# Performance work log

Measured on AMD Instinct MI355X. Metric: run time of the kernel, lower is better.

The kernel has to match this reference:

```python
import jax, jax.numpy as jnp
import numpy as np
from jax import lax

B, T, H, W, C = 32, 250, 28, 28, 1
CLASSES, IPC = 25, 10
UNITS = 512
MEM_CELLS = CLASSES * IPC  # 250
CELL = 64
HEADS = 4
FEAT = 2 * 2 * 32          # conv output flattened = 128
XDIM = FEAT + CLASSES      # 153
IN_LSTM = XDIM + HEADS * CELL  # 409
EPS_BN = 1e-3


def setup_inputs() -> dict:
    key = jax.random.key(0)
    ks = iter(jax.random.split(key, 40))
    s = 0.02
    d = {}
    d['images'] = jax.random.normal(next(ks), (B, T, H, W, C), jnp.float32)
    d['previous_labels'] = jax.random.randint(next(ks), (B, T), 0, CLASSES, jnp.int32)
    # conv stack
    for i, (ci, co) in enumerate([(1, 8), (8, 16), (16, 32)], start=1):
        d[f'k{i}'] = jax.random.normal(next(ks), (3, 3, ci, co), jnp.float32) * s
        d[f'cb{i}'] = jnp.zeros((co,), jnp.float32)
        d[f'g{i}'] = jnp.ones((co,), jnp.float32)
        d[f'be{i}'] = jnp.zeros((co,), jnp.float32)
        d[f'mm{i}'] = jnp.zeros((co,), jnp.float32)
        d[f'mv{i}'] = jnp.ones((co,), jnp.float32)
    # LSTM cell (keras gate order i,f,g,o)
    d['Wx'] = jax.random.normal(next(ks), (IN_LSTM, 4 * UNITS), jnp.float32) * s
    d['Wh'] = jax.random.normal(next(ks), (UNITS, 4 * UNITS), jnp.float32) * s
    d['bl'] = jnp.zeros((4 * UNITS,), jnp.float32)
    # parameters dense -> (read_heads+1)*cell_size, tanh
    d['Wp'] = jax.random.normal(next(ks), (UNITS, (HEADS + 1) * CELL), jnp.float32) * s
    d['bp'] = jnp.zeros(((HEADS + 1) * CELL,), jnp.float32)
    # output layer: Dense(units, tanh) on concat(h, read_value)
    d['Wo'] = jax.random.normal(next(ks), (UNITS + HEADS * CELL, UNITS), jnp.float32) * s
    d['bo'] = jnp.zeros((UNITS,), jnp.float32)
    # final classifier
    d['Wf'] = jax.random.normal(next(ks), (UNITS, CLASSES), jnp.float32) * s
    d['bf'] = jnp.zeros((CLASSES,), jnp.float32)
    return d


def _conv_bn_relu(x, k, cb, g, be, mm, mv):
    y = lax.conv_general_dilated(x, k, (2, 2), 'VALID',
                                 dimension_numbers=('NHWC', 'HWIO', 'NHWC')) + cb
    y = (y - mm) * g * lax.rsqrt(mv + EPS_BN) + be  # inference BN
    return jax.nn.relu(y)


def _l2n(x):
    return x * lax.rsqrt(jnp.maximum(jnp.sum(x * x, axis=-1, keepdims=True), 1e-12))


def _forward(images, previous_labels, k1, cb1, g1, be1, mm1, mv1,
             k2, cb2, g2, be2, mm2, mv2, k3, cb3, g3, be3, mm3, mv3,
             Wx, Wh, bl, Wp, bp, Wo, bo, Wf, bf):
    x = images.reshape(B * T, H, W, C)
    x = _conv_bn_relu(x, k1, cb1, g1, be1, mm1, mv1)
    x = _conv_bn_relu(x, k2, cb2, g2, be2, mm2, mv2)
    x = _conv_bn_relu(x, k3, cb3, g3, be3, mm3, mv3)
    x = x.reshape(B, T, FEAT)
    oh = jax.nn.one_hot(previous_labels, CLASSES, dtype=x.dtype)
    x = jnp.concatenate([x, oh], axis=-1)  # [B, T, XDIM]

    def step(carry, xt):
        h, c, rv, mem = carry
        inp = jnp.concatenate([xt, rv], axis=-1)
        z = inp @ Wx + h @ Wh + bl
        zi, zf, zg, zo = jnp.split(z, 4, axis=-1)
        i, f, g = jax.nn.sigmoid(zi), jax.nn.sigmoid(zf), jnp.tanh(zg)
        o = jax.nn.sigmoid(zo)
        c = f * c + i * g
        h = o * jnp.tanh(c)
        hid = jnp.tanh(h @ Wp + bp)
        wv = hid[:, :CELL]                                # write value
        keys = hid[:, CELL:].reshape(B, HEADS, CELL)
        att = jnp.einsum('brs,bms->brm', _l2n(keys), _l2n(mem))
        w = jax.nn.softmax(att, axis=-1)
        rv = jnp.einsum('brm,bms->brs', w, mem).reshape(B, HEADS * CELL)
        mem = jnp.concatenate([wv[:, None, :], mem[:, :-1]], axis=1)  # shift write
        out = jnp.tanh(jnp.concatenate([h, rv], axis=-1) @ Wo + bo)
        return (h, c, rv, mem), out

    carry0 = (jnp.zeros((B, UNITS)), jnp.zeros((B, UNITS)),
              jnp.zeros((B, HEADS * CELL)), jnp.zeros((B, MEM_CELLS, CELL)))
    _, ys = lax.scan(step, carry0, jnp.swapaxes(x, 0, 1))  # ys: [T, B, UNITS]
    rnn_out = jnp.swapaxes(ys, 0, 1)
    return jax.nn.softmax(rnn_out @ Wf + bf, axis=-1)


def reference(images, previous_labels, k1, cb1, g1, be1, mm1, mv1,
              k2, cb2, g2, be2, mm2, mv2, k3, cb3, g3, be3, mm3, mv3,
              Wx, Wh, bl, Wp, bp, Wo, bo, Wf, bf):
    return _forward(images, previous_labels, k1, cb1, g1, be1, mm1, mv1,
                    k2, cb2, g2, be2, mm2, mv2, k3, cb3, g3, be3, mm3, mv3,
                    Wx, Wh, bl, Wp, bp, Wo, bo, Wf, bf)
```

## Files before the change

### kernel.cpp

```cpp
#include <hip/hip_runtime.h>


constexpr size_t OFF_FEATP  = 0;
constexpr size_t OFF_WXI    = OFF_FEATP + (size_t)8000 * 128;
constexpr size_t OFF_WHI    = OFF_WXI + (size_t)409 * 2048;
constexpr size_t OFF_BLI    = OFF_WHI + (size_t)512 * 2048;
constexpr size_t OFF_ZP0    = OFF_BLI + 2048;
constexpr size_t OFF_ZP1    = OFF_ZP0 + 131072;
constexpr size_t OFF_OH0    = OFF_ZP1 + 131072;
constexpr size_t OFF_OH1    = OFF_OH0 + 32768;
constexpr size_t OFF_HP0    = OFF_OH1 + 32768;
constexpr size_t OFF_HP1    = OFF_HP0 + 10240;
constexpr size_t OFF_OUTPRE = OFF_HP1 + 10240;
constexpr size_t OFF_HT     = OFF_OUTPRE + 16384;
constexpr size_t OFF_RVT    = OFF_HT + 32768;
constexpr size_t OFF_BAR    = OFF_RVT + 16384;
constexpr size_t OFF_WPT    = OFF_BAR + 4096;
constexpr size_t WS_FLOATS  = OFF_WPT + (size_t)163840;

constexpr size_t OFF_HTT = OFF_ZP1;
constexpr size_t OFF_WVP = OFF_ZP1 + 32768;

constexpr int DYN_FLOATS = 34816;
constexpr int DYN_BYTES  = DYN_FLOATS * 4;

constexpr int CZP = 0, CHT = 512, COH = 1024, CWV = 1536, CRV = 2048,
              COP = 2560, CCO = 3072, CRING = 3584;

__device__ __forceinline__ float sigm(float x) { return 1.f / (1.f + __expf(-x)); }

__device__ __forceinline__ void st_sc(float* p, float v) {
  __hip_atomic_store(p, v, __ATOMIC_RELAXED, __HIP_MEMORY_SCOPE_AGENT);
}
__device__ __forceinline__ float ld_sc(const float* p) {
  return __hip_atomic_load(p, __ATOMIC_RELAXED, __HIP_MEMORY_SCOPE_AGENT);
}
__device__ __forceinline__ void ld8x2_sc(const double* b0, double* v) {
  const double *p0 = b0, *p1 = b0 + 512, *p2 = b0 + 1024, *p3 = b0 + 1536,
               *p4 = b0 + 2048, *p5 = b0 + 2560, *p6 = b0 + 3072, *p7 = b0 + 3584;
  asm volatile(
      "global_load_dwordx2 %0, %8, off sc0 sc1\n\t"
      "global_load_dwordx2 %1, %9, off sc0 sc1\n\t"
      "global_load_dwordx2 %2, %10, off sc0 sc1\n\t"
      "global_load_dwordx2 %3, %11, off sc0 sc1\n\t"
      "global_load_dwordx2 %4, %12, off sc0 sc1\n\t"
      "global_load_dwordx2 %5, %13, off sc0 sc1\n\t"
      "global_load_dwordx2 %6, %14, off sc0 sc1\n\t"
      "global_load_dwordx2 %7, %15, off sc0 sc1\n\t"
      "s_waitcnt vmcnt(0)"
      : "=&v"(v[0]), "=&v"(v[1]), "=&v"(v[2]), "=&v"(v[3]),
        "=&v"(v[4]), "=&v"(v[5]), "=&v"(v[6]), "=&v"(v[7])
      : "v"(p0), "v"(p1), "v"(p2), "v"(p3), "v"(p4), "v"(p5), "v"(p6), "v"(p7)
      : "memory");
}
__device__ __forceinline__ void ld10x2_sc(const double* b0, const double* z0,
                                          const double* z1, double* v) {
  const double *p0 = b0, *p1 = b0 + 512, *p2 = b0 + 1024, *p3 = b0 + 1536,
               *p4 = b0 + 2048, *p5 = b0 + 2560, *p6 = b0 + 3072, *p7 = b0 + 3584;
  asm volatile(
      "global_load_dwordx2 %0, %10, off sc0 sc1\n\t"
      "global_load_dwordx2 %1, %11, off sc0 sc1\n\t"
      "global_load_dwordx2 %2, %12, off sc0 sc1\n\t"
      "global_load_dwordx2 %3, %13, off sc0 sc1\n\t"
      "global_load_dwordx2 %4, %14, off sc0 sc1\n\t"
      "global_load_dwordx2 %5, %15, off sc0 sc1\n\t"
      "global_load_dwordx2 %6, %16, off sc0 sc1\n\t"
      "global_load_dwordx2 %7, %17, off sc0 sc1\n\t"
      "global_load_dwordx2 %8, %18, off sc0 sc1\n\t"
      "global_load_dwordx2 %9, %19, off sc0 sc1\n\t"
      "s_waitcnt vmcnt(0)"
      : "=&v"(v[0]), "=&v"(v[1]), "=&v"(v[2]), "=&v"(v[3]), "=&v"(v[4]),
        "=&v"(v[5]), "=&v"(v[6]), "=&v"(v[7]), "=&v"(v[8]), "=&v"(v[9])
      : "v"(p0), "v"(p1), "v"(p2), "v"(p3), "v"(p4), "v"(p5), "v"(p6), "v"(p7),
        "v"(z0), "v"(z1)
      : "memory");
}
__device__ __forceinline__ void ldpair_sc(const float* a, const float* b,
                                          float& x, float& y) {
  asm volatile(
      "global_load_dword %0, %2, off sc0 sc1\n\t"
      "global_load_dword %1, %3, off sc0 sc1\n\t"
      "s_waitcnt vmcnt(0)"
      : "=&v"(x), "=&v"(y) : "v"(a), "v"(b) : "memory");
}
__device__ __forceinline__ double ld1x2_sc(const double* a) {
  double x;
  asm volatile(
      "global_load_dwordx2 %0, %1, off sc0 sc1\n\t"
      "s_waitcnt vmcnt(0)"
      : "=&v"(x) : "v"(a) : "memory");
  return x;
}
__device__ __forceinline__ int sum8_bar(const int* b) {
  int v0, v1, v2, v3, v4, v5, v6, v7;
  asm volatile(
      "global_load_dword %0, %8, off sc0 sc1\n\t"
      "global_load_dword %1, %9, off sc0 sc1\n\t"
      "global_load_dword %2, %10, off sc0 sc1\n\t"
      "global_load_dword %3, %11, off sc0 sc1\n\t"
      "global_load_dword %4, %12, off sc0 sc1\n\t"
      "global_load_dword %5, %13, off sc0 sc1\n\t"
      "global_load_dword %6, %14, off sc0 sc1\n\t"
      "global_load_dword %7, %15, off sc0 sc1\n\t"
      "s_waitcnt vmcnt(0)"
      : "=&v"(v0), "=&v"(v1), "=&v"(v2), "=&v"(v3),
        "=&v"(v4), "=&v"(v5), "=&v"(v6), "=&v"(v7)
      : "v"(b), "v"(b + 64), "v"(b + 128), "v"(b + 192),
        "v"(b + 256), "v"(b + 320), "v"(b + 384), "v"(b + 448)
      : "memory");
  return ((v0 + v1) + (v2 + v3)) + ((v4 + v5) + (v6 + v7));
}

__global__ __launch_bounds__(256) void prep_kernel(const float* __restrict__ Wx,
                                                   const float* __restrict__ Wh,
                                                   const float* __restrict__ bl,
                                                   const float* __restrict__ Wp,
                                                   float* __restrict__ ws) {
  float* WXI = ws + OFF_WXI;
  float* WHI = ws + OFF_WHI;
  float* BLI = ws + OFF_BLI;
  float* WPT = ws + OFF_WPT;
  const int t0 = 409 * 2048;
  const int t1 = t0 + 512 * 2048;
  const int t2 = t1 + 2048;
  const int total = t2 + 163840;
  for (int idx = blockIdx.x * blockDim.x + threadIdx.x; idx < total;
       idx += gridDim.x * blockDim.x) {
    if (idx < t0) {
      int k = idx >> 11, cc = idx & 2047;
      WXI[idx] = Wx[(size_t)k * 2048 + (cc & 3) * 512 + (cc >> 2)];
    } else if (idx < t1) {
      int j = idx - t0;
      int k = j >> 11, cc = j & 2047;
      WHI[j] = Wh[(size_t)k * 2048 + (cc & 3) * 512 + (cc >> 2)];
    } else if (idx < t2) {
      int cc = idx - t1;
      BLI[cc] = bl[(cc & 3) * 512 + (cc >> 2)];
    } else {
      int e = idx - t2;
      int k4 = e / 1280, r = e - k4 * 1280;
      int j = r >> 2, ks = r & 3;
      WPT[e] = Wp[(size_t)(k4 * 4 + ks) * 320 + j];
    }
  }
}

__global__ __launch_bounds__(128) void conv_kernel(
    const float* __restrict__ img,
    const float* __restrict__ k1, const float* __restrict__ cb1, const float* __restrict__ g1,
    const float* __restrict__ be1, const float* __restrict__ mm1, const float* __restrict__ mv1,
    const float* __restrict__ k2, const float* __restrict__ cb2, const float* __restrict__ g2,
    const float* __restrict__ be2, const float* __restrict__ mm2, const float* __restrict__ mv2,
    const float* __restrict__ k3, const float* __restrict__ cb3, const float* __restrict__ g3,
    const float* __restrict__ be3, const float* __restrict__ mm3, const float* __restrict__ mv3,
    float* __restrict__ ws) {
  __shared__ float s_in[784];
  __shared__ float s_y1[13 * 13 * 8];
  __shared__ float s_y2[6 * 6 * 16];
  __shared__ float s_k1[72], s_k2[1152], s_k3[4608];
  __shared__ float s_s1[8], s_b1[8], s_s2[16], s_b2[16], s_s3[32], s_b3[32];
  float* FEATP = ws + OFF_FEATP;
  const int n = blockIdx.x, tid = threadIdx.x;
  const float* ip = img + (size_t)n * 784;
  for (int i = tid; i < 784; i += 128) s_in[i] = ip[i];
  for (int i = tid; i < 72; i += 128) s_k1[i] = k1[i];
  for (int i = tid; i < 1152; i += 128) s_k2[i] = k2[i];
  for (int i = tid; i < 4608; i += 128) s_k3[i] = k3[i];
  if (tid < 8) {
    float s = g1[tid] * rsqrtf(mv1[tid] + 1e-3f);
    s_s1[tid] = s; s_b1[tid] = (cb1[tid] - mm1[tid]) * s + be1[tid];
  } else if (tid >= 32 && tid < 48) {
    int c = tid - 32;
    float s = g2[c] * rsqrtf(mv2[c] + 1e-3f);
    s_s2[c] = s; s_b2[c] = (cb2[c] - mm2[c]) * s + be2[c];
  } else if (tid >= 64 && tid < 96) {
    int c = tid - 64;
    float s = g3[c] * rsqrtf(mv3[c] + 1e-3f);
    s_s3[c] = s; s_b3[c] = (cb3[c] - mm3[c]) * s + be3[c];
  }
  __syncthreads();
  for (int idx = tid; idx < 13 * 13 * 8; idx += 128) {
    int co = idx & 7, pos = idx >> 3;
    int j = pos % 13, i = pos / 13;
    float acc = 0.f;
    #pragma unroll
    for (int ky = 0; ky < 3; ++ky)
      #pragma unroll
      for (int kx = 0; kx < 3; ++kx)
        acc += s_in[(2 * i + ky) * 28 + (2 * j + kx)] * s_k1[(ky * 3 + kx) * 8 + co];
    float v = acc * s_s1[co] + s_b1[co];
    s_y1[idx] = v > 0.f ? v : 0.f;
  }
  __syncthreads();
  for (int idx = tid; idx < 6 * 6 * 16; idx += 128) {
    int co = idx & 15, pos = idx >> 4;
    int j = pos % 6, i = pos / 6;
    float acc = 0.f;
    for (int ky = 0; ky < 3; ++ky)
      for (int kx = 0; kx < 3; ++kx) {
        int base = ((2 * i + ky) * 13 + (2 * j + kx)) * 8;
        int kb = (ky * 3 + kx) * 128 + co;
        #pragma unroll
        for (int ci = 0; ci < 8; ++ci) acc += s_y1[base + ci] * s_k2[kb + ci * 16];
      }
    float v = acc * s_s2[co] + s_b2[co];
    s_y2[idx] = v > 0.f ? v : 0.f;
  }
  __syncthreads();
  for (int idx = tid; idx < 128; idx += 128) {
    int co = idx & 31, pos = idx >> 5;
    int j = pos & 1, i = pos >> 1;
    float acc = 0.f;
    for (int ky = 0; ky < 3; ++ky)
      for (int kx = 0; kx < 3; ++kx) {
        int base = ((2 * i + ky) * 6 + (2 * j + kx)) * 16;
        int kb = (ky * 3 + kx) * 512 + co;
        #pragma unroll
        for (int ci = 0; ci < 16; ++ci) acc += s_y2[base + ci] * s_k3[kb + ci * 32];
      }
    float v = acc * s_s3[co] + s_b3[co];
    FEATP[(size_t)n * 128 + idx] = v > 0.f ? v : 0.f;
  }
}

__global__ __launch_bounds__(512) void lstm_kernel(
    const int* __restrict__ labels,
    const float* __restrict__ Wo, const float* __restrict__ bo,
    const float* __restrict__ Wp, const float* __restrict__ bp,
    const float* __restrict__ Wf, const float* __restrict__ bf,
    float* __restrict__ ws, float* __restrict__ out) {
  extern __shared__ float dyn[];
  const float* FEATP = ws + OFF_FEATP;
  const float* WXI   = ws + OFF_WXI;
  const float* WHI   = ws + OFF_WHI;
  const float* BLI   = ws + OFF_BLI;
  float* ZP0    = ws + OFF_ZP0;
  float* OH0    = ws + OFF_OH0;
  float* OH1    = ws + OFF_OH1;
  float* OUTPRE = ws + OFF_OUTPRE;
  float* HT     = ws + OFF_HT;
  float* HTT    = ws + OFF_HTT;
  float* RVT    = ws + OFF_RVT;
  float* WVPp   = ws + OFF_WVP;
  const float* WPT = ws + OFF_WPT;
  int*   BARp   = (int*)(ws + OFF_BAR);

  const int bid = blockIdx.x;
  const int tid = threadIdx.x;

  auto waitC = [&](int base, int target) {
    if (tid == 0) {
      while (sum8_bar(BARp + base) < target) {}
    }
    __syncthreads();
  };
  auto bumpC = [&](int base) {
    asm volatile("s_waitcnt vmcnt(0)" ::: "memory");
    __syncthreads();
    if (tid == 0) atomicAdd(&BARp[base + ((bid & 7) << 6)], 1);
  };

  auto stage_act = [&](float* dst, const float* src) {
    double v[8];
    ld8x2_sc((const double*)src + tid, v);
    #pragma unroll
    for (int j = 0; j < 8; ++j) {
      int i = (tid + j * 512) << 1;
      *(double*)&dst[(i >> 5) * 36 + (i & 31)] = v[j];
    }
  };

  auto E32 = [&](const float* Wm, const float* Am, int K, float* part, float2& r) {
    const int wv = tid >> 6, l = tid & 63;
    const int ksub = l & 1, cg = (l >> 1) & 3, bg = l >> 3;
    const int Kp = K >> 4;
    const int kb = wv * (K >> 3) + ksub * Kp;
    const float* wp = Wm + (size_t)kb * 32 + cg * 8;
    const float* ap = Am + (size_t)kb * 36 + bg * 4;
    float4 acc[8];
    #pragma unroll
    for (int i = 0; i < 8; ++i) acc[i] = {0.f, 0.f, 0.f, 0.f};
    #pragma unroll 4
    for (int kk = 0; kk < Kp; ++kk) {
      float4 w0 = *(const float4*)(wp + kk * 32);
      float4 w1 = *(const float4*)(wp + kk * 32 + 4);
      float4 a  = *(const float4*)(ap + kk * 36);
      float wl[8];
      *(float4*)&wl[0] = w0; *(float4*)&wl[4] = w1;
      #pragma unroll
      for (int i = 0; i < 8; ++i) {
        acc[i].x = fmaf(wl[i], a.x, acc[i].x);
        acc[i].y = fmaf(wl[i], a.y, acc[i].y);
        acc[i].z = fmaf(wl[i], a.z, acc[i].z);
        acc[i].w = fmaf(wl[i], a.w, acc[i].w);
      }
    }
    #pragma unroll
    for (int i = 0; i < 8; ++i) {
      acc[i].x += __shfl_xor(acc[i].x, 1, 64);
      acc[i].y += __shfl_xor(acc[i].y, 1, 64);
      acc[i].z += __shfl_xor(acc[i].z, 1, 64);
      acc[i].w += __shfl_xor(acc[i].w, 1, 64);
    }
    const int ob = (cg * 8) * 36 + bg * 4;
    if (ksub == 0 && wv < 4) {
      float* pb = part + wv * 1152 + ob;
      #pragma unroll
      for (int i = 0; i < 8; ++i) *(float4*)(pb + i * 36) = acc[i];
    }
    __syncthreads();
    if (ksub == 0 && wv >= 4) {
      float* pb = part + (wv - 4) * 1152 + ob;
      #pragma unroll
      for (int i = 0; i < 8; ++i) {
        float4 t = *(float4*)(pb + i * 36);
        t.x += acc[i].x; t.y += acc[i].y; t.z += acc[i].z; t.w += acc[i].w;
        *(float4*)(pb + i * 36) = t;
      }
    }
    __syncthreads();
    const int c = tid & 31, b2 = (tid >> 5) * 2;
    const int o = c * 36 + b2;
    float2 s0 = *(float2*)(part + o);
    float2 s1 = *(float2*)(part + 1152 + o);
    float2 s2 = *(float2*)(part + 2304 + o);
    float2 s3 = *(float2*)(part + 3456 + o);
    r.x = (s0.x + s1.x) + (s2.x + s3.x);
    r.y = (s0.y + s1.y) + (s2.y + s3.y);
  };

  if (bid < 64) {
    const int c0 = bid * 32;
    for (int i = tid; i < 8192; i += 512)
      dyn[i] = WXI[(size_t)(153 + (i >> 5)) * 2048 + c0 + (i & 31)];
    for (int i = tid; i < 4096; i += 512)
      dyn[8192 + i] = WXI[(size_t)(i >> 5) * 2048 + c0 + (i & 31)];
    if (tid < 256) dyn[12288 + tid] = 0.f;
  } else if (bid < 80) {
    const int u0 = (bid - 64) * 32;
    for (int i = tid; i < 8192; i += 512)
      dyn[i] = Wo[(size_t)(512 + (i >> 5)) * 512 + u0 + (i & 31)];
    if (tid < 32) dyn[8192 + tid] = bo[u0 + tid];
  } else if (bid < 144) {
    const int c0 = (bid - 80) * 32;
    for (int i = tid; i < 16384; i += 512)
      dyn[i] = WHI[(size_t)(i >> 5) * 2048 + c0 + (i & 31)];
    if (tid < 32) dyn[16384 + tid] = BLI[c0 + tid];
  } else if (bid < 160) {
    const int u0 = (bid - 144) * 32;
    for (int i = tid; i < 8192; i += 512)
      dyn[i] = Wo[(size_t)(i >> 5) * 512 + u0 + (i & 31)];
  } else if (bid < 176) {
    const int u0 = (bid - 160) * 32;
    for (int i = tid; i < 8192; i += 512)
      dyn[i] = Wo[(size_t)(256 + (i >> 5)) * 512 + u0 + (i & 31)];
  } else if (bid < 240) {
    const int hp = (bid - 176) & 1;
    for (int i = tid; i < 17000; i += 512) dyn[i] = 0.f;
    if (tid < 256) dyn[17000 + tid] = rsqrtf(1e-12f);
    if (tid < 128) dyn[21264 + tid] = bp[64 + hp * 128 + tid];
    if (tid < 64)  dyn[21392 + tid] = bp[tid];
  } else if (bid < 244) {
    const int kh = (bid - 240) >> 1, cp = (bid - 240) & 1;
    for (int i = tid; i < 8192; i += 512) {
      int k = i >> 5, c = i & 31;
      dyn[i] = Wp[(size_t)(kh * 256 + k) * 320 + cp * 32 + c];
    }
  } else if (bid < 252) {
    for (int i = tid; i < 12800; i += 512) dyn[i] = Wf[i];
    if (tid < 25) dyn[12800 + tid] = bf[tid];
  }
  __syncthreads();

  auto azPre = [&](int t) {
    const int c0 = bid * 32;
    const float* zpS = ZP0 + (t & 1) * 65536;
    float* zf = dyn + 27392;
    const int bb = tid >> 4, c2 = tid & 15;
    double x = ld1x2_sc((const double*)(zpS + (size_t)bb * 2048 + c0) + c2);
    *(double*)&zf[bb * 32 + c2 * 2] = x;
  };
  auto azGatesMain = [&](int t) {
    const float* rvS = RVT + ((t + 1) & 1) * 8192;
    float* htD  = HT + (t & 1) * 16384;
    float* htD2 = HTT + (t & 1) * 16384;
    float* Wz = dyn; float* Cst = dyn + 12288; float* rvT = dyn + 12544;
    float* zx = dyn + 26368; float* zf = dyn + 27392; float* part = dyn + 28416;
    {
      double v[8];
      ld8x2_sc((const double*)rvS + tid, v);
      #pragma unroll
      for (int j = 0; j < 8; ++j) {
        int i = (tid + j * 512) << 1;
        *(double*)&rvT[(i >> 5) * 36 + (i & 31)] = v[j];
      }
    }
    __syncthreads();
    float2 r;
    E32(Wz, rvT, 256, part, r);
    const int c = tid & 31, b2 = (tid >> 5) * 2;
    zf[b2 * 32 + c] += r.x + zx[b2 * 32 + c];
    zf[(b2 + 1) * 32 + c] += r.y + zx[(b2 + 1) * 32 + c];
    __syncthreads();
    if (tid < 256) {
      int u = tid & 7, b = tid >> 3;
      float4 z = *(float4*)(zf + b * 32 + u * 4);
      float ig = sigm(z.x), fg = sigm(z.y), gg = tanhf(z.z), og = sigm(z.w);
      float cc = fg * Cst[b * 8 + u] + ig * gg;
      Cst[b * 8 + u] = cc;
      float hv = og * tanhf(cc);
      st_sc(&htD[(size_t)(bid * 8 + u) * 32 + b], hv);
      st_sc(&htD2[(size_t)b * 512 + bid * 8 + u], hv);
    }
  };
  auto azX = [&](int tt) {
    float* Wxx = dyn + 8192; float* xT = dyn + 21760;
    float* zx = dyn + 26368; float* part = dyn + 28416;
    for (int i = tid; i < 4096; i += 512) {
      int b = i >> 7, k = i & 127;
      xT[k * 36 + b] = FEATP[((size_t)b * 250 + tt) * 128 + k];
    }
    __syncthreads();
    float2 r;
    E32(Wxx, xT, 128, part, r);
    const int c = tid & 31, b2 = (tid >> 5) * 2;
    zx[b2 * 32 + c] = r.x;
    zx[(b2 + 1) * 32 + c] = r.y;
  };
  auto aoOut = [&](int t) {
    const int u0 = (bid - 64) * 32;
    const float* rvS  = RVT + ((t + 1) & 1) * 8192;
    const float* oh0S = OH0 + ((t + 1) & 1) * 16384;
    const float* oh1S = OH1 + ((t + 1) & 1) * 16384;
    float* W = dyn; float* bo_l = dyn + 8192; float* rvT = dyn + 8224;
    float* of = dyn + 17440; float* part = dyn + 18464;
    {
      const int b = tid >> 4, c2 = tid & 15;
      double v[10];
      ld10x2_sc((const double*)rvS + tid,
                (const double*)(oh0S + b * 512 + u0) + c2,
                (const double*)(oh1S + b * 512 + u0) + c2, v);
      #pragma unroll
      for (int j = 0; j < 8; ++j) {
        int i = (tid + j * 512) << 1;
        *(double*)&rvT[(i >> 5) * 36 + (i & 31)] = v[j];
      }
      float2 f0 = *(float2*)&v[8], f1 = *(float2*)&v[9];
      float2 s = {f0.x + f1.x, f0.y + f1.y};
      *(double*)&of[b * 32 + c2 * 2] = *(double*)&s;
    }
    __syncthreads();
    float2 r;
    E32(W, rvT, 256, part, r);
    const int c = tid & 31, b2 = (tid >> 5) * 2;
    float bv = bo_l[c];
    st_sc(&OUTPRE[b2 * 512 + u0 + c], r.x + of[b2 * 32 + c] + bv);
    st_sc(&OUTPRE[(b2 + 1) * 512 + u0 + c], r.y + of[(b2 + 1) * 32 + c] + bv);
  };
  auto zhLab = [&](int s) {
    __syncthreads();
    int* slab = (int*)(dyn + 16416);
    if (tid < 32) slab[tid] = labels[tid * 250 + s];
  };
  auto zhGemm = [&](int s) {
    const int c0 = (bid - 80) * 32;
    const float* htS = HT + ((s + 1) & 1) * 16384;
    float* zpD = ZP0 + (s & 1) * 65536;
    float* W = dyn; float* blc = dyn + 16384; int* slab = (int*)(dyn + 16416);
    float* A = dyn + 16448; float* part = dyn + 25664;
    stage_act(A, htS);
    __syncthreads();
    float2 r1;
    E32(W, A, 256, part, r1);
    __syncthreads();
    stage_act(A, htS + 8192);
    __syncthreads();
    float2 r2;
    E32(W + 8192, A, 256, part, r2);
    const int c = tid & 31, b2 = (tid >> 5) * 2;
    float base = blc[c];
    int l0 = slab[b2], l1 = slab[b2 + 1];
    st_sc(&zpD[(size_t)b2 * 2048 + c0 + c],
          r1.x + r2.x + base + WXI[(size_t)(128 + l0) * 2048 + c0 + c]);
    st_sc(&zpD[(size_t)(b2 + 1) * 2048 + c0 + c],
          r1.y + r2.y + base + WXI[(size_t)(128 + l1) * 2048 + c0 + c]);
  };
  auto p2Gemm = [&](int t) {
    const float* htBase = HT + (t & 1) * 16384;
    float* W = dyn; float* A = dyn + 8192; float* part = dyn + 17408;
    const bool isOLr = bid < 160;
    stage_act(A, isOLr ? htBase : (htBase + 8192));
    __syncthreads();
    float2 r;
    E32(W, A, 256, part, r);
    const int c = tid & 31, b2 = (tid >> 5) * 2;
    const int u0 = (isOLr ? (bid - 144) : (bid - 160)) * 32;
    float* d = (isOLr ? OH0 : OH1) + (t & 1) * 16384;
    st_sc(&d[b2 * 512 + u0 + c], r.x);
    st_sc(&d[(b2 + 1) * 512 + u0 + c], r.y);
  };
  auto caOutB = [&](int b, int t) {
    float* WfL = dyn; float* bfL = dyn + 12800;
    float* to = dyn + 12832; float* lp = dyn + 13344; float* lg = dyn + 13744;
    to[tid] = tanhf(ld_sc(&OUTPRE[b * 512 + tid]));
    __syncthreads();
    if (tid < 400) {
      int l = tid % 25, p = tid / 25;
      float s = 0.f;
      #pragma unroll
      for (int q = 0; q < 32; ++q) { int k = p * 32 + q; s += to[k] * WfL[k * 25 + l]; }
      lp[p * 25 + l] = s;
    }
    __syncthreads();
    if (tid < 25) {
      float s = bfL[tid];
      #pragma unroll
      for (int p = 0; p < 16; ++p) s += lp[p * 25 + tid];
      lg[tid] = s;
    }
    __syncthreads();
    if (tid == 0) {
      float mx = lg[0];
      for (int l = 1; l < 25; ++l) mx = fmaxf(mx, lg[l]);
      float ss = 0.f;
      for (int l = 0; l < 25; ++l) ss += __expf(lg[l] - mx);
      lg[25] = mx; lg[26] = 1.f / ss;
    }
    __syncthreads();
    if (tid < 25)
      out[((size_t)b * 250 + (t - 1)) * 25 + tid] = __expf(lg[tid] - lg[25]) * lg[26];
    __syncthreads();
  };

  if (bid < 64) {
    azX(0);
    for (int t = 0; t < 250; ++t) {
      waitC(CZP, 64 * (t + 1));
      azPre(t);
      if (t >= 2) {
        waitC(COH, 32 * (t - 1));
        waitC(CWV, 4 * (t - 1));
      }
      if (t >= 1) waitC(CRV, 64 * t);
      azGatesMain(t);
      bumpC(CHT);
      if (t < 249) azX(t + 1);
    }
  } else if (bid < 80) {
    for (int t = 1; t <= 250; ++t) {
      waitC(CRV, 64 * t);
      waitC(COH, 32 * t);
      if (t >= 2) waitC(CCO, 8 * (t - 1));
      aoOut(t);
      bumpC(COP);
    }
  } else if (bid < 144) {
    for (int s = 0; s < 250; ++s) {
      zhLab(s);
      if (s >= 1) waitC(CHT, 64 * s);
      zhGemm(s);
      bumpC(CZP);
    }
  } else if (bid < 176) {
    for (int t = 0; t < 250; ++t) {
      waitC(CHT, 64 * (t + 1));
      if (t >= 2) waitC(COP, 16 * (t - 1));
      p2Gemm(t);
      bumpC(COH);
    }
  } else if (bid < 240) {
    float* ring = dyn;
    float* rn   = dyn + 17000;
    float* h_s  = dyn + 17256;
    float* kpart= dyn + 17768;
    float* kv   = dyn + 18280;
    float* kn   = dyn + 18408;
    float* att  = dyn + 18536;
    float* redK = dyn + 19048;
    float* redM = dyn + 19052;
    float* redS = dyn + 19068;
    float* pslab= dyn + 19088;
    float* bpk  = dyn + 21264;
    float* bpw  = dyn + 21392;
    const int b = (bid - 176) >> 1, hp = (bid - 176) & 1;
    const int j = tid & 127, q = tid >> 7;
    const int J = 64 + hp * 128 + j;
    const float4* wbase = (const float4*)WPT + q * 32 * 320 + J;
    for (int t = 0; t < 250; ++t) {
      float4 pf[16];
      #pragma unroll
      for (int i = 0; i < 16; ++i) pf[i] = wbase[i * 320];
      waitC(CHT, 64 * (t + 1));
      if (t >= 2) waitC(COP, 16 * (t - 1));
      h_s[tid] = ld_sc(&HTT[(t & 1) * 16384 + b * 512 + tid]);
      __syncthreads();
      {
        float a = 0.f;
        #pragma unroll
        for (int i = 0; i < 16; ++i) {
          float4 h4 = *(const float4*)&h_s[q * 128 + i * 4];
          a += pf[i].x * h4.x + pf[i].y * h4.y + pf[i].z * h4.z + pf[i].w * h4.w;
        }
        #pragma unroll 4
        for (int i = 16; i < 32; ++i) {
          float4 w = wbase[i * 320];
          float4 h4 = *(const float4*)&h_s[q * 128 + i * 4];
          a += w.x * h4.x + w.y * h4.y + w.z * h4.z + w.w * h4.w;
        }
        kpart[q * 128 + j] = a;
      }
      __syncthreads();
      if (tid < 128) {
        float kr = kpart[tid] + kpart[128 + tid] + kpart[256 + tid] +
                   kpart[384 + tid] + bpk[tid];
        float v = tanhf(kr);
        kv[tid] = v;
        float pq = v * v;
        #pragma unroll
        for (int off = 32; off; off >>= 1) pq += __shfl_xor(pq, off, 64);
        if ((tid & 63) == 0) redK[tid >> 6] = rsqrtf(fmaxf(pq, 1e-12f));
      }
      __syncthreads();
      if (tid < 128) kn[tid] = kv[tid] * redK[tid >> 6];
      __syncthreads();
      const int start = (250 - t) % 250;
      const int m = tid >> 1, hh = tid & 1;
      {
        float v;
        if (m < 250) {
          int p = start + m; if (p >= 250) p -= 250;
          const float4* c4 = (const float4*)ring + p * 17;
          const float4* k4 = (const float4*)kn + hh * 16;
          float d = 0.f;
          #pragma unroll
          for (int s4 = 0; s4 < 16; ++s4) {
            float4 cc = c4[s4], kk = k4[s4];
            d += cc.x * kk.x + cc.y * kk.y + cc.z * kk.z + cc.w * kk.w;
          }
          v = d * rn[p];
        } else v = -3.0e38f;
        float mx = v;
        #pragma unroll
        for (int off = 2; off <= 32; off <<= 1) mx = fmaxf(mx, __shfl_xor(mx, off, 64));
        if ((tid & 63) < 2) redM[(tid >> 6) * 2 + (tid & 1)] = mx;
        __syncthreads();
        float MX = redM[hh];
        #pragma unroll
        for (int w = 1; w < 8; ++w) MX = fmaxf(MX, redM[w * 2 + hh]);
        float e = (m < 250) ? __expf(v - MX) : 0.f;
        if (m < 250) att[hh * 256 + m] = e;
        float sm = e;
        #pragma unroll
        for (int off = 2; off <= 32; off <<= 1) sm += __shfl_xor(sm, off, 64);
        if ((tid & 63) < 2) redS[(tid >> 6) * 2 + (tid & 1)] = sm;
      }
      __syncthreads();
      {
        int hh2 = tid >> 8, s4 = (tid >> 4) & 15, g = tid & 15;
        float4 a4 = {0.f, 0.f, 0.f, 0.f};
        for (int mm = g; mm < 250; mm += 16) {
          int p = start + mm; if (p >= 250) p -= 250;
          float w = att[hh2 * 256 + mm];
          float4 cc = ((const float4*)ring)[p * 17 + s4];
          a4.x = fmaf(w, cc.x, a4.x); a4.y = fmaf(w, cc.y, a4.y);
          a4.z = fmaf(w, cc.z, a4.z); a4.w = fmaf(w, cc.w, a4.w);
        }
        *(float4*)&pslab[(hh2 * 16 + s4) * 68 + g * 4] = a4;
      }
      __syncthreads();
      if (tid < 128) {
        int hh3 = tid >> 6, s = tid & 63;
        float denom = redS[hh3];
        #pragma unroll
        for (int w = 1; w < 8; ++w) denom += redS[w * 2 + hh3];
        float sum = 0.f;
        #pragma unroll
        for (int g = 0; g < 16; ++g)
          sum += pslab[(hh3 * 16 + (s >> 2)) * 68 + g * 4 + (s & 3)];
        float* rvD = RVT + (t & 1) * 8192;
        st_sc(&rvD[((2 * hp + hh3) * 64 + s) * 32 + b], sum / denom);
      }
      bumpC(CRV);
      waitC(CWV, 4 * (t + 1));
      {
        int ip = start + 249; if (ip >= 250) ip -= 250;
        if (tid < 64) {
          float p0, p1;
          ldpair_sc(&WVPp[(t & 1) * 4096 + b * 64 + tid],
                    &WVPp[(t & 1) * 4096 + 2048 + b * 64 + tid], p0, p1);
          float nv = tanhf(p0 + p1 + bpw[tid]);
          ring[ip * 68 + tid] = nv;
          float n2 = nv * nv;
          #pragma unroll
          for (int off = 32; off; off >>= 1) n2 += __shfl_xor(n2, off, 64);
          if (tid == 0) rn[ip] = rsqrtf(fmaxf(n2, 1e-12f));
        }
      }
      bumpC(CRING);
    }
  } else if (bid < 244) {
    const int kh = (bid - 240) >> 1, cp = (bid - 240) & 1;
    float* W = dyn; float* A = dyn + 8192; float* part = dyn + 17408;
    for (int t = 0; t < 250; ++t) {
      waitC(CHT, 64 * (t + 1));
      if (t >= 2) waitC(CRING, 64 * (t - 1));
      stage_act(A, HT + (t & 1) * 16384 + kh * 8192);
      __syncthreads();
      float2 r;
      E32(W, A, 256, part, r);
      const int c = tid & 31, b2 = (tid >> 5) * 2;
      float* d = WVPp + (t & 1) * 4096 + kh * 2048;
      st_sc(&d[b2 * 64 + cp * 32 + c], r.x);
      st_sc(&d[(b2 + 1) * 64 + cp * 32 + c], r.y);
      bumpC(CWV);
    }
  } else if (bid < 252) {
    const int b0 = (bid - 244) * 4;
    for (int t = 1; t <= 250; ++t) {
      waitC(COP, 16 * t);
      caOutB(b0 + 0, t);
      caOutB(b0 + 1, t);
      caOutB(b0 + 2, t);
      caOutB(b0 + 3, t);
      bumpC(CCO);
    }
  }
}

extern "C" void kernel_launch(void* const* d_in, const int* in_sizes, int n_in,
                              void* d_out, int out_size, void* d_ws, size_t ws_size,
                              hipStream_t stream) {
  const float* images = (const float*)d_in[0];
  const int* labels = (const int*)d_in[1];
  const float* k1  = (const float*)d_in[2];
  const float* cb1 = (const float*)d_in[3];
  const float* g1  = (const float*)d_in[4];
  const float* be1 = (const float*)d_in[5];
  const float* mm1 = (const float*)d_in[6];
  const float* mv1 = (const float*)d_in[7];
  const float* k2  = (const float*)d_in[8];
  const float* cb2 = (const float*)d_in[9];
  const float* g2  = (const float*)d_in[10];
  const float* be2 = (const float*)d_in[11];
  const float* mm2 = (const float*)d_in[12];
  const float* mv2 = (const float*)d_in[13];
  const float* k3  = (const float*)d_in[14];
  const float* cb3 = (const float*)d_in[15];
  const float* g3  = (const float*)d_in[16];
  const float* be3 = (const float*)d_in[17];
  const float* mm3 = (const float*)d_in[18];
  const float* mv3 = (const float*)d_in[19];
  const float* Wx  = (const float*)d_in[20];
  const float* Wh  = (const float*)d_in[21];
  const float* bl  = (const float*)d_in[22];
  const float* Wp  = (const float*)d_in[23];
  const float* bp  = (const float*)d_in[24];
  const float* Wo  = (const float*)d_in[25];
  const float* bo  = (const float*)d_in[26];
  const float* Wf  = (const float*)d_in[27];
  const float* bf  = (const float*)d_in[28];
  float* ws = (float*)d_ws;

  hipFuncSetAttribute((const void*)lstm_kernel,
                      hipFuncAttributeMaxDynamicSharedMemorySize, DYN_BYTES);

  hipMemsetAsync((char*)d_ws + OFF_ZP0 * sizeof(float), 0,
                 (WS_FLOATS - OFF_ZP0) * sizeof(float), stream);
  prep_kernel<<<1024, 256, 0, stream>>>(Wx, Wh, bl, Wp, ws);
  conv_kernel<<<8000, 128, 0, stream>>>(images,
      k1, cb1, g1, be1, mm1, mv1,
      k2, cb2, g2, be2, mm2, mv2,
      k3, cb3, g3, be3, mm3, mv3, ws);
  lstm_kernel<<<256, 512, DYN_BYTES, stream>>>(labels, Wo, bo, Wp, bp, Wf, bf, ws,
                                               (float*)d_out);
}
```

Before: 4.684 ms.

## Replace counter barriers with tagged value-flag pairs for producer-consumer sync

Each inter-block data value is now stored as a 64-bit (value, step-tag) pair, and consumers spin on the tags of the data they read instead of waiting on global atomic counter barriers. This removes several waitC/bumpC round trips per timestep (CZP, CHT, CRV, CWV), so consumers can start as soon as their own inputs land. The cost is twice the workspace traffic and footprint for the activations, plus polling loads with s_sleep that can retry full 16-byte vectors. The workspace memset now covers only the tagged buffers and the barrier region.

Result: faster. 3.935 ms (-16.0%).

```diff
diff --git a/kernel.cpp b/kernel.cpp
--- a/kernel.cpp
+++ b/kernel.cpp
@@ -5,91 +5,110 @@
 constexpr size_t OFF_WXI    = OFF_FEATP + (size_t)8000 * 128;
 constexpr size_t OFF_WHI    = OFF_WXI + (size_t)409 * 2048;
 constexpr size_t OFF_BLI    = OFF_WHI + (size_t)512 * 2048;
-constexpr size_t OFF_ZP0    = OFF_BLI + 2048;
-constexpr size_t OFF_ZP1    = OFF_ZP0 + 131072;
-constexpr size_t OFF_OH0    = OFF_ZP1 + 131072;
-constexpr size_t OFF_OH1    = OFF_OH0 + 32768;
-constexpr size_t OFF_HP0    = OFF_OH1 + 32768;
-constexpr size_t OFF_HP1    = OFF_HP0 + 10240;
-constexpr size_t OFF_OUTPRE = OFF_HP1 + 10240;
-constexpr size_t OFF_HT     = OFF_OUTPRE + 16384;
-constexpr size_t OFF_RVT    = OFF_HT + 32768;
-constexpr size_t OFF_BAR    = OFF_RVT + 16384;
+constexpr size_t OFF_ZP2    = OFF_BLI + 2048;
+constexpr size_t OFF_OH2A   = OFF_ZP2 + 262144;
+constexpr size_t OFF_OH2B   = OFF_OH2A + 65536;
+constexpr size_t OFF_OUTPRE2= OFF_OH2B + 65536;
+constexpr size_t OFF_HT2    = OFF_OUTPRE2 + 32768;
+constexpr size_t OFF_HTT2   = OFF_HT2 + 65536;
+constexpr size_t OFF_RVT2   = OFF_HTT2 + 65536;
+constexpr size_t OFF_WVP2   = OFF_RVT2 + 32768;
+constexpr size_t OFF_BAR    = OFF_WVP2 + 16384;
 constexpr size_t OFF_WPT    = OFF_BAR + 4096;
 constexpr size_t WS_FLOATS  = OFF_WPT + (size_t)163840;
 
-constexpr size_t OFF_HTT = OFF_ZP1;
-constexpr size_t OFF_WVP = OFF_ZP1 + 32768;
-
 constexpr int DYN_FLOATS = 34816;
 constexpr int DYN_BYTES  = DYN_FLOATS * 4;
 
-constexpr int CZP = 0, CHT = 512, COH = 1024, CWV = 1536, CRV = 2048,
-              COP = 2560, CCO = 3072, CRING = 3584;
+constexpr int COH = 0, COP = 512, CCO = 1024, CRING = 1536;
 
 __device__ __forceinline__ float sigm(float x) { return 1.f / (1.f + __expf(-x)); }
 
-__device__ __forceinline__ void st_sc(float* p, float v) {
-  __hip_atomic_store(p, v, __ATOMIC_RELAXED, __HIP_MEMORY_SCOPE_AGENT);
-}
-__device__ __forceinline__ float ld_sc(const float* p) {
-  return __hip_atomic_load(p, __ATOMIC_RELAXED, __HIP_MEMORY_SCOPE_AGENT);
-}
-__device__ __forceinline__ void ld8x2_sc(const double* b0, double* v) {
-  const double *p0 = b0, *p1 = b0 + 512, *p2 = b0 + 1024, *p3 = b0 + 1536,
-               *p4 = b0 + 2048, *p5 = b0 + 2560, *p6 = b0 + 3072, *p7 = b0 + 3584;
+typedef int iv2 __attribute__((ext_vector_type(2)));
+typedef int iv4 __attribute__((ext_vector_type(4)));
+
+__device__ __forceinline__ void st_pair(float* base, size_t pidx, float v, int tag) {
+  unsigned long long u = (unsigned long long)__float_as_uint(v) |
+                         ((unsigned long long)(unsigned)tag << 32);
+  __hip_atomic_store((unsigned long long*)(base + 2 * pidx), u,
+                     __ATOMIC_RELAXED, __HIP_MEMORY_SCOPE_AGENT);
+}
+__device__ __forceinline__ float spin_pair(const float* base, size_t pidx, int tag) {
+  const iv2* p = (const iv2*)(base + 2 * pidx);
+  iv2 v;
+  for (;;) {
+    asm volatile("global_load_dwordx2 %0, %1, off sc0 sc1\n\ts_waitcnt vmcnt(0)"
+                 : "=&v"(v) : "v"(p) : "memory");
+    if (v[1] == tag) break;
+    __builtin_amdgcn_s_sleep(1);
+  }
+  return __int_as_float(v[0]);
+}
+__device__ __forceinline__ float2 spin_pair2(const float* base, size_t pidx, int tag) {
+  const iv4* p = (const iv4*)(base + 2 * pidx);
+  iv4 v;
+  for (;;) {
+    asm volatile("global_load_dwordx4 %0, %1, off sc0 sc1\n\ts_waitcnt vmcnt(0)"
+                 : "=&v"(v) : "v"(p) : "memory");
+    if (v[1] == tag && v[3] == tag) break;
+    __builtin_amdgcn_s_sleep(1);
+  }
+  return {__int_as_float(v[0]), __int_as_float(v[2])};
+}
+__device__ __forceinline__ float2 spin_pair_2addr(const float* a, const float* b, int tag) {
+  const iv2* pa = (const iv2*)a;
+  const iv2* pb = (const iv2*)b;
+  iv2 x, y;
+  for (;;) {
+    asm volatile(
+        "global_load_dwordx2 %0, %2, off sc0 sc1\n\t"
+        "global_load_dwordx2 %1, %3, off sc0 sc1\n\t"
+        "s_waitcnt vmcnt(0)"
+        : "=&v"(x), "=&v"(y) : "v"(pa), "v"(pb) : "memory");
+    if (x[1] == tag && y[1] == tag) break;
+    __builtin_amdgcn_s_sleep(1);
+  }
+  return {__int_as_float(x[0]), __int_as_float(y[0])};
+}
+__device__ __forceinline__ void ld8i4_sc(const iv4* b0, iv4* v) {
+  const iv4 *p0 = b0, *p1 = b0 + 512, *p2 = b0 + 1024, *p3 = b0 + 1536,
+            *p4 = b0 + 2048, *p5 = b0 + 2560, *p6 = b0 + 3072, *p7 = b0 + 3584;
   asm volatile(
-      "global_load_dwordx2 %0, %8, off sc0 sc1\n\t"
-      "global_load_dwordx2 %1, %9, off sc0 sc1\n\t"
-      "global_load_dwordx2 %2, %10, off sc0 sc1\n\t"
-      "global_load_dwordx2 %3, %11, off sc0 sc1\n\t"
-      "global_load_dwordx2 %4, %12, off sc0 sc1\n\t"
-      "global_load_dwordx2 %5, %13, off sc0 sc1\n\t"
-      "global_load_dwordx2 %6, %14, off sc0 sc1\n\t"
-      "global_load_dwordx2 %7, %15, off sc0 sc1\n\t"
+      "global_load_dwordx4 %0, %8, off sc0 sc1\n\t"
+      "global_load_dwordx4 %1, %9, off sc0 sc1\n\t"
+      "global_load_dwordx4 %2, %10, off sc0 sc1\n\t"
+      "global_load_dwordx4 %3, %11, off sc0 sc1\n\t"
+      "global_load_dwordx4 %4, %12, off sc0 sc1\n\t"
+      "global_load_dwordx4 %5, %13, off sc0 sc1\n\t"
+      "global_load_dwordx4 %6, %14, off sc0 sc1\n\t"
+      "global_load_dwordx4 %7, %15, off sc0 sc1\n\t"
       "s_waitcnt vmcnt(0)"
       : "=&v"(v[0]), "=&v"(v[1]), "=&v"(v[2]), "=&v"(v[3]),
         "=&v"(v[4]), "=&v"(v[5]), "=&v"(v[6]), "=&v"(v[7])
       : "v"(p0), "v"(p1), "v"(p2), "v"(p3), "v"(p4), "v"(p5), "v"(p6), "v"(p7)
       : "memory");
 }
-__device__ __forceinline__ void ld10x2_sc(const double* b0, const double* z0,
-                                          const double* z1, double* v) {
-  const double *p0 = b0, *p1 = b0 + 512, *p2 = b0 + 1024, *p3 = b0 + 1536,
-               *p4 = b0 + 2048, *p5 = b0 + 2560, *p6 = b0 + 3072, *p7 = b0 + 3584;
+__device__ __forceinline__ void ld10i4_sc(const iv4* b0, const iv4* z0,
+                                          const iv4* z1, iv4* v) {
+  const iv4 *p0 = b0, *p1 = b0 + 512, *p2 = b0 + 1024, *p3 = b0 + 1536,
+            *p4 = b0 + 2048, *p5 = b0 + 2560, *p6 = b0 + 3072, *p7 = b0 + 3584;
   asm volatile(
-      "global_load_dwordx2 %0, %10, off sc0 sc1\n\t"
-      "global_load_dwordx2 %1, %11, off sc0 sc1\n\t"
-      "global_load_dwordx2 %2, %12, off sc0 sc1\n\t"
-      "global_load_dwordx2 %3, %13, off sc0 sc1\n\t"
-      "global_load_dwordx2 %4, %14, off sc0 sc1\n\t"
-      "global_load_dwordx2 %5, %15, off sc0 sc1\n\t"
-      "global_load_dwordx2 %6, %16, off sc0 sc1\n\t"
-      "global_load_dwordx2 %7, %17, off sc0 sc1\n\t"
-      "global_load_dwordx2 %8, %18, off sc0 sc1\n\t"
-      "global_load_dwordx2 %9, %19, off sc0 sc1\n\t"
+      "global_load_dwordx4 %0, %10, off sc0 sc1\n\t"
+      "global_load_dwordx4 %1, %11, off sc0 sc1\n\t"
+      "global_load_dwordx4 %2, %12, off sc0 sc1\n\t"
+      "global_load_dwordx4 %3, %13, off sc0 sc1\n\t"
+      "global_load_dwordx4 %4, %14, off sc0 sc1\n\t"
+      "global_load_dwordx4 %5, %15, off sc0 sc1\n\t"
+      "global_load_dwordx4 %6, %16, off sc0 sc1\n\t"
+      "global_load_dwordx4 %7, %17, off sc0 sc1\n\t"
+      "global_load_dwordx4 %8, %18, off sc0 sc1\n\t"
+      "global_load_dwordx4 %9, %19, off sc0 sc1\n\t"
       "s_waitcnt vmcnt(0)"
       : "=&v"(v[0]), "=&v"(v[1]), "=&v"(v[2]), "=&v"(v[3]), "=&v"(v[4]),
         "=&v"(v[5]), "=&v"(v[6]), "=&v"(v[7]), "=&v"(v[8]), "=&v"(v[9])
       : "v"(p0), "v"(p1), "v"(p2), "v"(p3), "v"(p4), "v"(p5), "v"(p6), "v"(p7),
         "v"(z0), "v"(z1)
       : "memory");
-}
-__device__ __forceinline__ void ldpair_sc(const float* a, const float* b,
-                                          float& x, float& y) {
-  asm volatile(
-      "global_load_dword %0, %2, off sc0 sc1\n\t"
-      "global_load_dword %1, %3, off sc0 sc1\n\t"
-      "s_waitcnt vmcnt(0)"
-      : "=&v"(x), "=&v"(y) : "v"(a), "v"(b) : "memory");
-}
-__device__ __forceinline__ double ld1x2_sc(const double* a) {
-  double x;
-  asm volatile(
-      "global_load_dwordx2 %0, %1, off sc0 sc1\n\t"
-      "s_waitcnt vmcnt(0)"
-      : "=&v"(x) : "v"(a) : "memory");
-  return x;
 }
 __device__ __forceinline__ int sum8_bar(const int* b) {
   int v0, v1, v2, v3, v4, v5, v6, v7;
@@ -234,14 +253,14 @@
   const float* WXI   = ws + OFF_WXI;
   const float* WHI   = ws + OFF_WHI;
   const float* BLI   = ws + OFF_BLI;
-  float* ZP0    = ws + OFF_ZP0;
-  float* OH0    = ws + OFF_OH0;
-  float* OH1    = ws + OFF_OH1;
-  float* OUTPRE = ws + OFF_OUTPRE;
-  float* HT     = ws + OFF_HT;
-  float* HTT    = ws + OFF_HTT;
-  float* RVT    = ws + OFF_RVT;
-  float* WVPp   = ws + OFF_WVP;
+  float* ZP2    = ws + OFF_ZP2;
+  float* OH2A   = ws + OFF_OH2A;
+  float* OH2B   = ws + OFF_OH2B;
+  float* OUTPRE2= ws + OFF_OUTPRE2;
+  float* HT2    = ws + OFF_HT2;
+  float* HTT2   = ws + OFF_HTT2;
+  float* RVT2   = ws + OFF_RVT2;
+  float* WVP2   = ws + OFF_WVP2;
   const float* WPT = ws + OFF_WPT;
   int*   BARp   = (int*)(ws + OFF_BAR);
 
@@ -260,13 +279,22 @@
     if (tid == 0) atomicAdd(&BARp[base + ((bid & 7) << 6)], 1);
   };
 
-  auto stage_act = [&](float* dst, const float* src) {
-    double v[8];
-    ld8x2_sc((const double*)src + tid, v);
+  auto stageP = [&](float* dst, const float* srcPairs, int tag) {
+    const iv4* sp = (const iv4*)srcPairs + tid;
+    iv4 v[8];
+    for (;;) {
+      ld8i4_sc(sp, v);
+      bool ok = true;
+      #pragma unroll
+      for (int j = 0; j < 8; ++j) ok = ok && (v[j][1] == tag) && (v[j][3] == tag);
+      if (ok) break;
+      __builtin_amdgcn_s_sleep(2);
+    }
     #pragma unroll
     for (int j = 0; j < 8; ++j) {
       int i = (tid + j * 512) << 1;
-      *(double*)&dst[(i >> 5) * 36 + (i & 31)] = v[j];
+      float2 f = {__int_as_float(v[j][0]), __int_as_float(v[j][2])};
+      *(float2*)&dst[(i >> 5) * 36 + (i & 31)] = f;
     }
   };
 
@@ -374,27 +402,17 @@
 
   auto azPre = [&](int t) {
     const int c0 = bid * 32;
-    const float* zpS = ZP0 + (t & 1) * 65536;
+    const float* zpP = ZP2 + (t & 1) * 131072;
     float* zf = dyn + 27392;
     const int bb = tid >> 4, c2 = tid & 15;
-    double x = ld1x2_sc((const double*)(zpS + (size_t)bb * 2048 + c0) + c2);
-    *(double*)&zf[bb * 32 + c2 * 2] = x;
+    float2 x = spin_pair2(zpP, (size_t)bb * 2048 + c0 + c2 * 2, t + 1);
+    *(float2*)&zf[bb * 32 + c2 * 2] = x;
   };
   auto azGatesMain = [&](int t) {
-    const float* rvS = RVT + ((t + 1) & 1) * 8192;
-    float* htD  = HT + (t & 1) * 16384;
-    float* htD2 = HTT + (t & 1) * 16384;
+    const float* rvP = RVT2 + ((t + 1) & 1) * 16384;
     float* Wz = dyn; float* Cst = dyn + 12288; float* rvT = dyn + 12544;
     float* zx = dyn + 26368; float* zf = dyn + 27392; float* part = dyn + 28416;
-    {
-      double v[8];
-      ld8x2_sc((const double*)rvS + tid, v);
-      #pragma unroll
-      for (int j = 0; j < 8; ++j) {
-        int i = (tid + j * 512) << 1;
-        *(double*)&rvT[(i >> 5) * 36 + (i & 31)] = v[j];
-      }
-    }
+    stageP(rvT, rvP, t);
     __syncthreads();
     float2 r;
     E32(Wz, rvT, 256, part, r);
@@ -409,8 +427,8 @@
       float cc = fg * Cst[b * 8 + u] + ig * gg;
       Cst[b * 8 + u] = cc;
       float hv = og * tanhf(cc);
-      st_sc(&htD[(size_t)(bid * 8 + u) * 32 + b], hv);
-      st_sc(&htD2[(size_t)b * 512 + bid * 8 + u], hv);
+      st_pair(HT2 + (t & 1) * 32768, (size_t)(bid * 8 + u) * 32 + b, hv, t + 1);
+      st_pair(HTT2 + (t & 1) * 32768, (size_t)b * 512 + bid * 8 + u, hv, t + 1);
     }
   };
   auto azX = [&](int tt) {
@@ -429,33 +447,42 @@
   };
   auto aoOut = [&](int t) {
     const int u0 = (bid - 64) * 32;
-    const float* rvS  = RVT + ((t + 1) & 1) * 8192;
-    const float* oh0S = OH0 + ((t + 1) & 1) * 16384;
-    const float* oh1S = OH1 + ((t + 1) & 1) * 16384;
+    const float* rvP  = RVT2 + ((t + 1) & 1) * 16384;
+    const float* ohaP = OH2A + ((t + 1) & 1) * 32768;
+    const float* ohbP = OH2B + ((t + 1) & 1) * 32768;
     float* W = dyn; float* bo_l = dyn + 8192; float* rvT = dyn + 8224;
     float* of = dyn + 17440; float* part = dyn + 18464;
     {
       const int b = tid >> 4, c2 = tid & 15;
-      double v[10];
-      ld10x2_sc((const double*)rvS + tid,
-                (const double*)(oh0S + b * 512 + u0) + c2,
-                (const double*)(oh1S + b * 512 + u0) + c2, v);
+      const iv4* rp = (const iv4*)rvP + tid;
+      const iv4* za = (const iv4*)ohaP + (b * 256 + (u0 >> 1) + c2);
+      const iv4* zb = (const iv4*)ohbP + (b * 256 + (u0 >> 1) + c2);
+      iv4 v[10];
+      for (;;) {
+        ld10i4_sc(rp, za, zb, v);
+        bool ok = true;
+        #pragma unroll
+        for (int j = 0; j < 10; ++j) ok = ok && (v[j][1] == t) && (v[j][3] == t);
+        if (ok) break;
+        __builtin_amdgcn_s_sleep(2);
+      }
       #pragma unroll
       for (int j = 0; j < 8; ++j) {
         int i = (tid + j * 512) << 1;
-        *(double*)&rvT[(i >> 5) * 36 + (i & 31)] = v[j];
-      }
-      float2 f0 = *(float2*)&v[8], f1 = *(float2*)&v[9];
-      float2 s = {f0.x + f1.x, f0.y + f1.y};
-      *(double*)&of[b * 32 + c2 * 2] = *(double*)&s;
+        float2 f = {__int_as_float(v[j][0]), __int_as_float(v[j][2])};
+        *(float2*)&rvT[(i >> 5) * 36 + (i & 31)] = f;
+      }
+      float2 s = {__int_as_float(v[8][0]) + __int_as_float(v[9][0]),
+                  __int_as_float(v[8][2]) + __int_as_float(v[9][2])};
+      *(float2*)&of[b * 32 + c2 * 2] = s;
     }
     __syncthreads();
     float2 r;
     E32(W, rvT, 256, part, r);
     const int c = tid & 31, b2 = (tid >> 5) * 2;
     float bv = bo_l[c];
-    st_sc(&OUTPRE[b2 * 512 + u0 + c], r.x + of[b2 * 32 + c] + bv);
-    st_sc(&OUTPRE[(b2 + 1) * 512 + u0 + c], r.y + of[(b2 + 1) * 32 + c] + bv);
+    st_pair(OUTPRE2, (size_t)b2 * 512 + u0 + c, r.x + of[b2 * 32 + c] + bv, t);
+    st_pair(OUTPRE2, (size_t)(b2 + 1) * 512 + u0 + c, r.y + of[(b2 + 1) * 32 + c] + bv, t);
   };
   auto zhLab = [&](int s) {
     __syncthreads();
@@ -464,45 +491,45 @@
   };
   auto zhGemm = [&](int s) {
     const int c0 = (bid - 80) * 32;
-    const float* htS = HT + ((s + 1) & 1) * 16384;
-    float* zpD = ZP0 + (s & 1) * 65536;
+    const float* htP = HT2 + ((s + 1) & 1) * 32768;
+    float* zpD = ZP2 + (s & 1) * 131072;
     float* W = dyn; float* blc = dyn + 16384; int* slab = (int*)(dyn + 16416);
     float* A = dyn + 16448; float* part = dyn + 25664;
-    stage_act(A, htS);
+    stageP(A, htP, s);
     __syncthreads();
     float2 r1;
     E32(W, A, 256, part, r1);
     __syncthreads();
-    stage_act(A, htS + 8192);
+    stageP(A, htP + 16384, s);
     __syncthreads();
     float2 r2;
     E32(W + 8192, A, 256, part, r2);
     const int c = tid & 31, b2 = (tid >> 5) * 2;
     float base = blc[c];
     int l0 = slab[b2], l1 = slab[b2 + 1];
-    st_sc(&zpD[(size_t)b2 * 2048 + c0 + c],
-          r1.x + r2.x + base + WXI[(size_t)(128 + l0) * 2048 + c0 + c]);
-    st_sc(&zpD[(size_t)(b2 + 1) * 2048 + c0 + c],
-          r1.y + r2.y + base + WXI[(size_t)(128 + l1) * 2048 + c0 + c]);
+    st_pair(zpD, (size_t)b2 * 2048 + c0 + c,
+            r1.x + r2.x + base + WXI[(size_t)(128 + l0) * 2048 + c0 + c], s + 1);
+    st_pair(zpD, (size_t)(b2 + 1) * 2048 + c0 + c,
+            r1.y + r2.y + base + WXI[(size_t)(128 + l1) * 2048 + c0 + c], s + 1);
   };
   auto p2Gemm = [&](int t) {
-    const float* htBase = HT + (t & 1) * 16384;
+    const float* htP = HT2 + (t & 1) * 32768;
     float* W = dyn; float* A = dyn + 8192; float* part = dyn + 17408;
     const bool isOLr = bid < 160;
-    stage_act(A, isOLr ? htBase : (htBase + 8192));
+    stageP(A, isOLr ? htP : (htP + 16384), t + 1);
     __syncthreads();
     float2 r;
     E32(W, A, 256, part, r);
     const int c = tid & 31, b2 = (tid >> 5) * 2;
     const int u0 = (isOLr ? (bid - 144) : (bid - 160)) * 32;
-    float* d = (isOLr ? OH0 : OH1) + (t & 1) * 16384;
-    st_sc(&d[b2 * 512 + u0 + c], r.x);
-    st_sc(&d[(b2 + 1) * 512 + u0 + c], r.y);
+    float* d = (isOLr ? OH2A : OH2B) + (t & 1) * 32768;
+    st_pair(d, (size_t)b2 * 512 + u0 + c, r.x, t + 1);
+    st_pair(d, (size_t)(b2 + 1) * 512 + u0 + c, r.y, t + 1);
   };
   auto caOutB = [&](int b, int t) {
     float* WfL = dyn; float* bfL = dyn + 12800;
     float* to = dyn + 12832; float* lp = dyn + 13344; float* lg = dyn + 13744;
-    to[tid] = tanhf(ld_sc(&OUTPRE[b * 512 + tid]));
+    to[tid] = tanhf(spin_pair(OUTPRE2, (size_t)b * 512 + tid, t));
     __syncthreads();
     if (tid < 400) {
       int l = tid % 25, p = tid / 25;
@@ -535,21 +562,13 @@
   if (bid < 64) {
     azX(0);
     for (int t = 0; t < 250; ++t) {
-      waitC(CZP, 64 * (t + 1));
       azPre(t);
-      if (t >= 2) {
-        waitC(COH, 32 * (t - 1));
-        waitC(CWV, 4 * (t - 1));
-      }
-      if (t >= 1) waitC(CRV, 64 * t);
+      if (t >= 2) waitC(COH, 32 * (t - 1));
       azGatesMain(t);
-      bumpC(CHT);
       if (t < 249) azX(t + 1);
     }
   } else if (bid < 80) {
     for (int t = 1; t <= 250; ++t) {
-      waitC(CRV, 64 * t);
-      waitC(COH, 32 * t);
       if (t >= 2) waitC(CCO, 8 * (t - 1));
       aoOut(t);
       bumpC(COP);
@@ -557,13 +576,10 @@
   } else if (bid < 144) {
     for (int s = 0; s < 250; ++s) {
       zhLab(s);
-      if (s >= 1) waitC(CHT, 64 * s);
       zhGemm(s);
-      bumpC(CZP);
     }
   } else if (bid < 176) {
     for (int t = 0; t < 250; ++t) {
-      waitC(CHT, 64 * (t + 1));
       if (t >= 2) waitC(COP, 16 * (t - 1));
       p2Gemm(t);
       bumpC(COH);
@@ -590,9 +606,8 @@
       float4 pf[16];
       #pragma unroll
       for (int i = 0; i < 16; ++i) pf[i] = wbase[i * 320];
-      waitC(CHT, 64 * (t + 1));
       if (t >= 2) waitC(COP, 16 * (t - 1));
-      h_s[tid] = ld_sc(&HTT[(t & 1) * 16384 + b * 512 + tid]);
+      h_s[tid] = spin_pair(HTT2 + (t & 1) * 32768, (size_t)b * 512 + tid, t + 1);
       __syncthreads();
       {
         float a = 0.f;
@@ -677,18 +692,17 @@
         #pragma unroll
         for (int g = 0; g < 16; ++g)
           sum += pslab[(hh3 * 16 + (s >> 2)) * 68 + g * 4 + (s & 3)];
-        float* rvD = RVT + (t & 1) * 8192;
-        st_sc(&rvD[((2 * hp + hh3) * 64 + s) * 32 + b], sum / denom);
-      }
-      bumpC(CRV);
-      waitC(CWV, 4 * (t + 1));
+        st_pair(RVT2 + (t & 1) * 16384,
+                (size_t)((2 * hp + hh3) * 64 + s) * 32 + b, sum / denom, t + 1);
+      }
+      __syncthreads();
       {
         int ip = start + 249; if (ip >= 250) ip -= 250;
         if (tid < 64) {
-          float p0, p1;
-          ldpair_sc(&WVPp[(t & 1) * 4096 + b * 64 + tid],
-                    &WVPp[(t & 1) * 4096 + 2048 + b * 64 + tid], p0, p1);
-          float nv = tanhf(p0 + p1 + bpw[tid]);
+          float2 p01 = spin_pair_2addr(
+              WVP2 + (t & 1) * 8192 + 2 * ((size_t)b * 64 + tid),
+              WVP2 + (t & 1) * 8192 + 4096 + 2 * ((size_t)b * 64 + tid), t + 1);
+          float nv = tanhf(p01.x + p01.y + bpw[tid]);
           ring[ip * 68 + tid] = nv;
           float n2 = nv * nv;
           #pragma unroll
@@ -702,22 +716,19 @@
     const int kh = (bid - 240) >> 1, cp = (bid - 240) & 1;
     float* W = dyn; float* A = dyn + 8192; float* part = dyn + 17408;
     for (int t = 0; t < 250; ++t) {
-      waitC(CHT, 64 * (t + 1));
       if (t >= 2) waitC(CRING, 64 * (t - 1));
-      stage_act(A, HT + (t & 1) * 16384 + kh * 8192);
+      stageP(A, HT2 + (t & 1) * 32768 + kh * 16384, t + 1);
       __syncthreads();
       float2 r;
       E32(W, A, 256, part, r);
       const int c = tid & 31, b2 = (tid >> 5) * 2;
-      float* d = WVPp + (t & 1) * 4096 + kh * 2048;
-      st_sc(&d[b2 * 64 + cp * 32 + c], r.x);
-      st_sc(&d[(b2 + 1) * 64 + cp * 32 + c], r.y);
-      bumpC(CWV);
+      float* d = WVP2 + (t & 1) * 8192 + kh * 4096;
+      st_pair(d, (size_t)b2 * 64 + cp * 32 + c, r.x, t + 1);
+      st_pair(d, (size_t)(b2 + 1) * 64 + cp * 32 + c, r.y, t + 1);
     }
   } else if (bid < 252) {
     const int b0 = (bid - 244) * 4;
     for (int t = 1; t <= 250; ++t) {
-      waitC(COP, 16 * t);
       caOutB(b0 + 0, t);
       caOutB(b0 + 1, t);
       caOutB(b0 + 2, t);
@@ -764,8 +775,8 @@
   hipFuncSetAttribute((const void*)lstm_kernel,
                       hipFuncAttributeMaxDynamicSharedMemorySize, DYN_BYTES);
 
-  hipMemsetAsync((char*)d_ws + OFF_ZP0 * sizeof(float), 0,
-                 (WS_FLOATS - OFF_ZP0) * sizeof(float), stream);
+  hipMemsetAsync((char*)d_ws + OFF_ZP2 * sizeof(float), 0,
+                 (OFF_WPT - OFF_ZP2) * sizeof(float), stream);
   prep_kernel<<<1024, 256, 0, stream>>>(Wx, Wh, bl, Wp, ws);
   conv_kernel<<<8000, 128, 0, stream>>>(images,
       k1, cb1, g1, be1, mm1, mv1,
```
